# Performance work log

Hardware: AMD Instinct MI355X
Metric: run time of the kernel (lower is better)

## Reference

```python
import jax, jax.numpy as jnp
import numpy as np

DIM = 2048
N_HEADS = 16
Q_LORA = 1536
KV_LORA = 512
NOPE = 128
ROPE = 64
V_DIM = 128
B, T = 1, 3072
EPS = 1e-6


def rmsnorm(x, w):
    var = jnp.mean(jnp.square(x), axis=-1, keepdims=True)
    return x * jax.lax.rsqrt(var + EPS) * w


def apply_rope(x, cos, sin):
    # x: (B, T, H, d); cos/sin: (T, d//2) -> broadcast (1, T, 1, d//2)
    c = cos[None, :, None, :]
    s = sin[None, :, None, :]
    x1 = x[..., 0::2]
    x2 = x[..., 1::2]
    r1 = x1 * c - x2 * s
    r2 = x1 * s + x2 * c
    return jnp.stack([r1, r2], axis=-1).reshape(x.shape)


def setup_inputs() -> dict:
    key = jax.random.key(0)
    ks = jax.random.split(key, 10)
    std = 0.02
    x = jax.random.normal(ks[0], (B, T, DIM), dtype=jnp.float32)
    # RoPE angles: position * inv_freq, shape (T, ROPE//2)
    inv_freq = 1.0 / (10000.0 ** (np.arange(0, ROPE, 2, dtype=np.float32) / ROPE))
    freqs = jnp.asarray(np.arange(T, dtype=np.float32)[:, None] * inv_freq[None, :])
    # additive causal mask (T, T)
    mask = jnp.where(jnp.tril(jnp.ones((T, T), dtype=bool)), 0.0, -jnp.inf).astype(jnp.float32)
    wq_down = jax.random.normal(ks[1], (DIM, Q_LORA), dtype=jnp.float32) * std
    q_norm_w = jnp.ones((Q_LORA,), dtype=jnp.float32)
    wq_nope = jax.random.normal(ks[2], (Q_LORA, N_HEADS * NOPE), dtype=jnp.float32) * std
    wq_rope = jax.random.normal(ks[3], (Q_LORA, N_HEADS * ROPE), dtype=jnp.float32) * std
    wkv_down = jax.random.normal(ks[4], (DIM, KV_LORA + ROPE), dtype=jnp.float32) * std
    kv_norm_w = jnp.ones((KV_LORA,), dtype=jnp.float32)
    wkv_up = jax.random.normal(ks[5], (KV_LORA, N_HEADS * (NOPE + V_DIM)), dtype=jnp.float32) * std
    wo = jax.random.normal(ks[6], (N_HEADS * V_DIM, DIM), dtype=jnp.float32) * std
    return {
        'x': x, 'freqs': freqs, 'mask': mask,
        'wq_down': wq_down, 'q_norm_w': q_norm_w, 'wq_nope': wq_nope,
        'wq_rope': wq_rope, 'wkv_down': wkv_down, 'kv_norm_w': kv_norm_w,
        'wkv_up': wkv_up, 'wo': wo,
    }


def reference(x, freqs, mask, wq_down, q_norm_w, wq_nope, wq_rope,
              wkv_down, kv_norm_w, wkv_up, wo):
    cos, sin = jnp.cos(freqs), jnp.sin(freqs)
    # Q path: down-project, RMSNorm, split nope/rope heads
    q_lat = rmsnorm(x @ wq_down, q_norm_w)                      # (B,T,Q_LORA)
    q_nope = (q_lat @ wq_nope).reshape(B, T, N_HEADS, NOPE)
    q_rope = apply_rope((q_lat @ wq_rope).reshape(B, T, N_HEADS, ROPE), cos, sin)
    q = jnp.concatenate([q_nope, q_rope], axis=-1)              # (B,T,H,192)
    # KV path: joint down-projection -> latent c_kv + raw rope key
    kvd = x @ wkv_down                                          # (B,T,KV_LORA+ROPE)
    c_kv = kvd[..., :KV_LORA]
    k_rope_raw = kvd[..., KV_LORA:]                             # (B,T,ROPE)
    k_rope = jnp.broadcast_to(k_rope_raw[:, :, None, :], (B, T, N_HEADS, ROPE))
    k_rope = apply_rope(k_rope, cos, sin)
    kv_up = (rmsnorm(c_kv, kv_norm_w) @ wkv_up).reshape(B, T, N_HEADS, NOPE + V_DIM)
    k_nope = kv_up[..., :NOPE]
    v = kv_up[..., NOPE:]                                       # (B,T,H,V_DIM)
    k = jnp.concatenate([k_nope, k_rope], axis=-1)              # (B,T,H,192)
    scale = (NOPE + ROPE) ** (-0.5)
    attn = jnp.einsum('bqhd,bkhd->bhqk', q, k) * scale + mask[None, None]
    attn = jax.nn.softmax(attn, axis=-1)                        # dropout p=0 (eval)
    out = jnp.einsum('bhqk,bkhd->bqhd', attn, v).reshape(B, T, N_HEADS * V_DIM)
    return out @ wo                                             # (B,T,DIM)
```

## Files before the change

kernel.cpp:

```cpp
#include <hip/hip_runtime.h>
#include <hip/hip_bf16.h>

typedef __bf16 bf16_t;
typedef __bf16 bf16x8 __attribute__((ext_vector_type(8)));
typedef float f32x4 __attribute__((ext_vector_type(4)));

#define T_SEQ 3072
#define DIM 2048
#define NH 16
#define QLORA 1536
#define KVLORA 512
#define NOPE 128
#define ROPE 64
#define VDIM 128
#define HD 192
#define SCALE 0.07216878364870323f
#define CHUNK 12

#define T1KV_LD 2112
#define QNR_LD 3072

__device__ inline float wave_reduce_sum(float v) {
    #pragma unroll
    for (int off = 32; off > 0; off >>= 1) v += __shfl_down(v, off);
    return v;
}

__device__ inline float block_reduce_sum_256(float v) {
    __shared__ float red[4];
    int lane = threadIdx.x & 63, w = threadIdx.x >> 6;
    v = wave_reduce_sum(v);
    if (lane == 0) red[w] = v;
    __syncthreads();
    if (threadIdx.x == 0) red[0] = red[0] + red[1] + red[2] + red[3];
    __syncthreads();
    return red[0];
}

__device__ inline void glds16(const bf16_t* g, bf16_t* l) {
    __builtin_amdgcn_global_load_lds(
        (const __attribute__((address_space(1))) unsigned int*)g,
        (__attribute__((address_space(3))) unsigned int*)l, 16, 0, 0);
}

__global__ void f2b_kernel(const float* __restrict__ in, bf16_t* __restrict__ out, int n) {
    int i = (blockIdx.x * 256 + threadIdx.x) * 4;
    if (i < n) {
        float4 v = *(const float4*)&in[i];
        bf16_t o[4] = {(bf16_t)v.x, (bf16_t)v.y, (bf16_t)v.z, (bf16_t)v.w};
        *(uint2*)&out[i] = *(const uint2*)o;
    }
}

__global__ __launch_bounds__(256) void transp_kernel(
    const float* __restrict__ in, bf16_t* __restrict__ out, int K, int N)
{
    __shared__ float tile[32][33];
    int k0 = blockIdx.y * 32, n0 = blockIdx.x * 32;
    int tx = threadIdx.x & 31, ty = threadIdx.x >> 5;
    #pragma unroll
    for (int i = 0; i < 4; ++i)
        tile[ty + i * 8][tx] = in[(size_t)(k0 + ty + i * 8) * N + n0 + tx];
    __syncthreads();
    #pragma unroll
    for (int i = 0; i < 4; ++i)
        out[(size_t)(n0 + ty + i * 8) * K + k0 + tx] = (bf16_t)tile[tx][ty + i * 8];
}

__global__ __launch_bounds__(256) void vt_transp(
    const bf16_t* __restrict__ kvu, bf16_t* __restrict__ vt)
{
    __shared__ bf16_t tile[32][34];
    int t0 = blockIdx.x * 32, d0 = blockIdx.y * 32, h = blockIdx.z;
    int tx = threadIdx.x & 31, ty = threadIdx.x >> 5;
    #pragma unroll
    for (int i = 0; i < 4; ++i)
        tile[ty + i * 8][tx] = kvu[(size_t)(t0 + ty + i * 8) * (NH * 256) + h * 256 + NOPE + d0 + tx];
    __syncthreads();
    #pragma unroll
    for (int i = 0; i < 4; ++i)
        vt[((size_t)h * VDIM + d0 + ty + i * 8) * T_SEQ + t0 + tx] = tile[tx][ty + i * 8];
}

__global__ __launch_bounds__(256) void gemm_mfma(
    const bf16_t* __restrict__ A, const bf16_t* __restrict__ Bt,
    float* __restrict__ Cf, bf16_t* __restrict__ Cb,
    int M, int N, int K, int lda, int ldb, int ldc, int writef)
{
    __shared__ __align__(16) bf16_t As[2][128 * 32];
    __shared__ __align__(16) bf16_t Bs[2][128 * 32];
    int tid = threadIdx.x;
    int w = tid >> 6, lane = tid & 63;
    int quad = lane >> 4, l16 = lane & 15;
    int bm = blockIdx.y * 128, bn = blockIdx.x * 128;
    int wm = (w & 1) * 64, wn = (w >> 1) * 64;

    int srow = tid >> 2, soff = (tid & 3) * 8;
    const bf16_t* a0 = A + (size_t)(bm + srow) * lda + soff;
    const bf16_t* a1 = A + (size_t)(bm + 64 + srow) * lda + soff;
    int br0 = bn + srow;      if (br0 >= N) br0 = N - 1;
    int br1 = bn + 64 + srow; if (br1 >= N) br1 = N - 1;
    const bf16_t* b0 = Bt + (size_t)br0 * ldb + soff;
    const bf16_t* b1 = Bt + (size_t)br1 * ldb + soff;

    f32x4 acc[4][4];
    #pragma unroll
    for (int i = 0; i < 4; ++i)
        #pragma unroll
        for (int j = 0; j < 4; ++j)
            acc[i][j] = (f32x4){0.f, 0.f, 0.f, 0.f};

    int nk = K >> 5;
    glds16(a0, &As[0][tid * 8]);
    glds16(a1, &As[0][tid * 8 + 2048]);
    glds16(b0, &Bs[0][tid * 8]);
    glds16(b1, &Bs[0][tid * 8 + 2048]);
    a0 += 32; a1 += 32; b0 += 32; b1 += 32;

    for (int t = 0; t < nk; ++t) {
        int cur = t & 1;
        if (t + 1 < nk) {
            int nxt = cur ^ 1;
            glds16(a0, &As[nxt][tid * 8]);
            glds16(a1, &As[nxt][tid * 8 + 2048]);
            glds16(b0, &Bs[nxt][tid * 8]);
            glds16(b1, &Bs[nxt][tid * 8 + 2048]);
            a0 += 32; a1 += 32; b0 += 32; b1 += 32;
            asm volatile("s_waitcnt vmcnt(4)" ::: "memory");
        } else {
            asm volatile("s_waitcnt vmcnt(0)" ::: "memory");
        }
        __builtin_amdgcn_s_barrier();
        __builtin_amdgcn_sched_barrier(0);

        bf16x8 af[4], bfr[4];
        #pragma unroll
        for (int t4 = 0; t4 < 4; ++t4) {
            af[t4]  = *(const bf16x8*)&As[cur][(wm + t4 * 16 + l16) * 32 + quad * 8];
            bfr[t4] = *(const bf16x8*)&Bs[cur][(wn + t4 * 16 + l16) * 32 + quad * 8];
        }
        #pragma unroll
        for (int i = 0; i < 4; ++i)
            #pragma unroll
            for (int j = 0; j < 4; ++j)
                acc[i][j] = __builtin_amdgcn_mfma_f32_16x16x32_bf16(af[i], bfr[j], acc[i][j], 0, 0, 0);

        __builtin_amdgcn_sched_barrier(0);
        __builtin_amdgcn_s_barrier();
        __builtin_amdgcn_sched_barrier(0);
    }

    #pragma unroll
    for (int i = 0; i < 4; ++i) {
        #pragma unroll
        for (int j = 0; j < 4; ++j) {
            #pragma unroll
            for (int r = 0; r < 4; ++r) {
                int row = bm + wm + i * 16 + quad * 4 + r;
                int col = bn + wn + j * 16 + l16;
                if (col < N) {
                    if (writef) Cf[(size_t)row * ldc + col] = acc[i][j][r];
                    else        Cb[(size_t)row * ldc + col] = (bf16_t)acc[i][j][r];
                }
            }
        }
    }
}

__global__ __launch_bounds__(256) void rmsnorm_rows(
    bf16_t* __restrict__ X, const float* __restrict__ w, int N, int ld)
{
    int row = blockIdx.x;
    bf16_t* x = X + (size_t)row * ld;
    float ss = 0.f;
    for (int i = threadIdx.x; i < N; i += 256) { float v = (float)x[i]; ss += v * v; }
    ss = block_reduce_sum_256(ss);
    float sc = rsqrtf(ss / (float)N + 1e-6f);
    for (int i = threadIdx.x; i < N; i += 256)
        x[i] = (bf16_t)((float)x[i] * sc * w[i]);
}

__global__ __launch_bounds__(256) void kv_post(
    const bf16_t* __restrict__ kvd, const float* __restrict__ w,
    const float* __restrict__ freqs,
    bf16_t* __restrict__ ckvn, bf16_t* __restrict__ kr)
{
    int row = blockIdx.x;
    const bf16_t* src = kvd + (size_t)row * T1KV_LD;
    float ss = 0.f;
    for (int i = threadIdx.x; i < KVLORA; i += 256) { float v = (float)src[i]; ss += v * v; }
    ss = block_reduce_sum_256(ss);
    float sc = rsqrtf(ss / (float)KVLORA + 1e-6f);
    for (int i = threadIdx.x; i < KVLORA; i += 256)
        ckvn[(size_t)row * KVLORA + i] = (bf16_t)((float)src[i] * sc * w[i]);
    if (threadIdx.x < 32) {
        int i = threadIdx.x;
        float f = freqs[row * 32 + i];
        float c = cosf(f), s = sinf(f);
        float x1 = (float)src[KVLORA + 2 * i], x2 = (float)src[KVLORA + 2 * i + 1];
        kr[(size_t)row * ROPE + 2 * i]     = (bf16_t)(x1 * c - x2 * s);
        kr[(size_t)row * ROPE + 2 * i + 1] = (bf16_t)(x1 * s + x2 * c);
    }
}

__global__ void rope_q(bf16_t* __restrict__ qr, const float* __restrict__ freqs) {
    int idx = blockIdx.x * 256 + threadIdx.x;
    if (idx >= T_SEQ * NH * 32) return;
    int t = idx >> 9;
    int rem = idx & 511;
    int h = rem >> 5;
    int i = rem & 31;
    float f = freqs[t * 32 + i];
    float c = cosf(f), s = sinf(f);
    bf16_t* p = qr + (size_t)t * QNR_LD + h * ROPE + 2 * i;
    float x1 = (float)p[0], x2 = (float)p[1];
    p[0] = (bf16_t)(x1 * c - x2 * s);
    p[1] = (bf16_t)(x1 * s + x2 * c);
}

#define P_STRIDE 72
__global__ __launch_bounds__(256, 2) void attn_v10(
    const bf16_t* __restrict__ QNR,
    const bf16_t* __restrict__ KVU, const bf16_t* __restrict__ KR,
    const bf16_t* __restrict__ Vt,
    bf16_t* __restrict__ Opart, float* __restrict__ lpart)
{
    __shared__ __align__(16) bf16_t Kn[64 * 128];
    __shared__ __align__(16) bf16_t Kr[64 * 64];
    __shared__ __align__(16) bf16_t Vs[128 * 64];
    __shared__ __align__(16) bf16_t Ps[4][32 * P_STRIDE];

    int qt2 = blockIdx.x, cx = blockIdx.y, h = blockIdx.z;
    int ktmax = 2 * qt2 + 2;
    int kt0 = cx * CHUNK;
    if (kt0 >= ktmax) return;
    int kt1 = min(ktmax, kt0 + CHUNK);
    int g = qt2 / 6, r6 = qt2 - g * 6;
    int slot = h * 60 + 3 * g * (g + 1) + r6 * (g + 1) + cx;

    int tid = threadIdx.x;
    int w = tid >> 6, lane = tid & 63;
    int quad = lane >> 4, l16 = lane & 15;
    int qbase = qt2 * 128;

    bf16x8 qf[2][6];
    #pragma unroll
    for (int qs = 0; qs < 2; ++qs) {
        int qrow = qbase + qs * 64 + w * 16 + l16;
        #pragma unroll
        for (int kk = 0; kk < 4; ++kk)
            qf[qs][kk] = *(const bf16x8*)&QNR[(size_t)qrow * QNR_LD + h * NOPE + kk * 32 + quad * 8];
        #pragma unroll
        for (int kk = 4; kk < 6; ++kk)
            qf[qs][kk] = *(const bf16x8*)&QNR[(size_t)qrow * QNR_LD + (NH * NOPE) + h * ROPE + (kk - 4) * 32 + quad * 8];
    }

    int l4 = lane >> 4, l3 = lane >> 3;
    const bf16_t* kn_e = KVU + (size_t)(kt0 * 64 + w * 16 + l4) * (NH * 256) + h * 256 + ((lane & 15) ^ l4) * 8;
    const bf16_t* kn_o = KVU + (size_t)(kt0 * 64 + w * 16 + l4) * (NH * 256) + h * 256 + ((lane & 15) ^ (4 + l4)) * 8;
    const bf16_t* krp  = KR  + (size_t)(kt0 * 64 + w * 16 + l3) * ROPE + ((lane & 7) ^ l3) * 8;
    const bf16_t* vp   = Vt  + ((size_t)h * VDIM + w * 32 + l3) * T_SEQ + kt0 * 64 + ((lane & 7) ^ l3) * 8;

    bf16x8 ones;
    #pragma unroll
    for (int i = 0; i < 8; ++i) ones[i] = (bf16_t)1.0f;

    f32x4 o[2][8];
    #pragma unroll
    for (int qs = 0; qs < 2; ++qs)
        #pragma unroll
        for (int nt = 0; nt < 8; ++nt) o[qs][nt] = (f32x4){0.f, 0.f, 0.f, 0.f};
    f32x4 lacc[2];
    lacc[0] = (f32x4){0.f, 0.f, 0.f, 0.f};
    lacc[1] = (f32x4){0.f, 0.f, 0.f, 0.f};

    for (int kt = kt0; kt < kt1; ++kt) {
        int kbase = kt * 64;
        #pragma unroll
        for (int i = 0; i < 4; ++i)
            glds16(((i & 1) ? kn_o : kn_e) + (size_t)i * 4 * (NH * 256), &Kn[(w * 4 + i) * 512]);
        #pragma unroll
        for (int i = 0; i < 2; ++i)
            glds16(krp + (size_t)i * 8 * ROPE, &Kr[(w * 2 + i) * 512]);
        #pragma unroll
        for (int i = 0; i < 4; ++i)
            glds16(vp + (size_t)i * 8 * T_SEQ, &Vs[(w * 4 + i) * 512]);
        kn_e += (size_t)64 * NH * 256;
        kn_o += (size_t)64 * NH * 256;
        krp  += 64 * ROPE;
        vp   += 64;
        __syncthreads();

        f32x4 S[2][4];
        #pragma unroll
        for (int qs = 0; qs < 2; ++qs)
            #pragma unroll
            for (int c = 0; c < 4; ++c) S[qs][c] = (f32x4){0.f, 0.f, 0.f, 0.f};
        #pragma unroll
        for (int kk = 0; kk < 4; ++kk) {
            #pragma unroll
            for (int c = 0; c < 4; ++c) {
                bf16x8 kf = *(const bf16x8*)&Kn[(c * 16 + l16) * 128 + (((kk * 4 + quad) ^ (l16 & 7)) * 8)];
                S[0][c] = __builtin_amdgcn_mfma_f32_16x16x32_bf16(qf[0][kk], kf, S[0][c], 0, 0, 0);
                S[1][c] = __builtin_amdgcn_mfma_f32_16x16x32_bf16(qf[1][kk], kf, S[1][c], 0, 0, 0);
            }
        }
        #pragma unroll
        for (int kk = 4; kk < 6; ++kk) {
            #pragma unroll
            for (int c = 0; c < 4; ++c) {
                bf16x8 kf = *(const bf16x8*)&Kr[(c * 16 + l16) * 64 + ((((kk - 4) * 4 + quad) ^ (l16 & 7)) * 8)];
                S[0][c] = __builtin_amdgcn_mfma_f32_16x16x32_bf16(qf[0][kk], kf, S[0][c], 0, 0, 0);
                S[1][c] = __builtin_amdgcn_mfma_f32_16x16x32_bf16(qf[1][kk], kf, S[1][c], 0, 0, 0);
            }
        }

        #pragma unroll
        for (int qs = 0; qs < 2; ++qs) {
            #pragma unroll
            for (int c = 0; c < 4; ++c) {
                #pragma unroll
                for (int j = 0; j < 4; ++j) {
                    int col = kbase + c * 16 + l16;
                    int grow = qbase + qs * 64 + w * 16 + quad * 4 + j;
                    float p = (col <= grow) ? __expf(S[qs][c][j] * SCALE) : 0.f;
                    Ps[w][(qs * 16 + quad * 4 + j) * P_STRIDE + c * 16 + l16] = (bf16_t)p;
                }
            }
        }
        __asm__ volatile("s_waitcnt lgkmcnt(0)" ::: "memory");

        bf16x8 pf[2][2];
        #pragma unroll
        for (int qs = 0; qs < 2; ++qs) {
            pf[qs][0] = *(const bf16x8*)&Ps[w][(qs * 16 + l16) * P_STRIDE + quad * 8];
            pf[qs][1] = *(const bf16x8*)&Ps[w][(qs * 16 + l16) * P_STRIDE + 32 + quad * 8];
            lacc[qs] = __builtin_amdgcn_mfma_f32_16x16x32_bf16(pf[qs][0], ones, lacc[qs], 0, 0, 0);
            lacc[qs] = __builtin_amdgcn_mfma_f32_16x16x32_bf16(pf[qs][1], ones, lacc[qs], 0, 0, 0);
        }

        #pragma unroll
        for (int kk2 = 0; kk2 < 2; ++kk2) {
            #pragma unroll
            for (int nt = 0; nt < 8; ++nt) {
                bf16x8 vf = *(const bf16x8*)&Vs[(nt * 16 + l16) * 64 + (((kk2 * 4 + quad) ^ (l16 & 7)) * 8)];
                o[0][nt] = __builtin_amdgcn_mfma_f32_16x16x32_bf16(pf[0][kk2], vf, o[0][nt], 0, 0, 0);
                o[1][nt] = __builtin_amdgcn_mfma_f32_16x16x32_bf16(pf[1][kk2], vf, o[1][nt], 0, 0, 0);
            }
        }
        __syncthreads();
    }

    #pragma unroll
    for (int qs = 0; qs < 2; ++qs) {
        #pragma unroll
        for (int nt = 0; nt < 8; ++nt)
            #pragma unroll
            for (int j = 0; j < 4; ++j)
                Opart[(size_t)slot * 16384 + (qs * 64 + w * 16 + quad * 4 + j) * 128 + nt * 16 + l16] = (bf16_t)o[qs][nt][j];
        if (l16 == 0) {
            #pragma unroll
            for (int j = 0; j < 4; ++j)
                lpart[slot * 128 + qs * 64 + w * 16 + quad * 4 + j] = lacc[qs][j];
        }
    }
}

__global__ __launch_bounds__(512) void attn_combine(
    const bf16_t* __restrict__ Opart, const float* __restrict__ lpart,
    bf16_t* __restrict__ AO)
{
    int qt2 = blockIdx.x, h = blockIdx.y;
    int g = qt2 / 6, r6 = qt2 - g * 6;
    int nch = g + 1;
    int base = h * 60 + 3 * g * (g + 1) + r6 * (g + 1);
    int r = threadIdx.x >> 2, c0 = (threadIdx.x & 3) * 32;

    float acc[32];
    #pragma unroll
    for (int i = 0; i < 32; ++i) acc[i] = 0.f;
    float lsum = 0.f;
    for (int ch = 0; ch < nch; ++ch) {
        int slot = base + ch;
        const bf16_t* p = &Opart[(size_t)slot * 16384 + r * 128 + c0];
        #pragma unroll
        for (int v = 0; v < 4; ++v) {
            bf16x8 u = *(const bf16x8*)&p[v * 8];
            #pragma unroll
            for (int e = 0; e < 8; ++e) acc[v * 8 + e] += (float)u[e];
        }
        lsum += lpart[slot * 128 + r];
    }
    float inv = 1.0f / lsum;
    bf16_t* dst = AO + (size_t)(qt2 * 128 + r) * (NH * VDIM) + h * VDIM + c0;
    #pragma unroll
    for (int v = 0; v < 4; ++v) {
        bf16_t tmp[8];
        #pragma unroll
        for (int e = 0; e < 8; ++e) tmp[e] = (bf16_t)(acc[v * 8 + e] * inv);
        *(uint4*)&dst[v * 8] = *(const uint4*)tmp;
    }
}

extern "C" void kernel_launch(void* const* d_in, const int* in_sizes, int n_in,
                              void* d_out, int out_size, void* d_ws, size_t ws_size,
                              hipStream_t stream) {
    const float* x        = (const float*)d_in[0];
    const float* freqs    = (const float*)d_in[1];
    const float* wq_down  = (const float*)d_in[3];
    const float* q_norm_w = (const float*)d_in[4];
    const float* wq_nope  = (const float*)d_in[5];
    const float* wq_rope  = (const float*)d_in[6];
    const float* wkv_down = (const float*)d_in[7];
    const float* kv_norm_w= (const float*)d_in[8];
    const float* wkv_up   = (const float*)d_in[9];
    const float* wo       = (const float*)d_in[10];
    float* out = (float*)d_out;

    bf16_t* ws = (bf16_t*)d_ws;
    bf16_t* xb     = ws;
    bf16_t* wqd_t  = xb     + 6291456;
    bf16_t* wkvd_t = wqd_t  + 3145728;
    bf16_t* wqn_t  = wkvd_t + 1179648;
    bf16_t* wqr_t  = wqn_t  + 3145728;
    bf16_t* wkvu_t = wqr_t  + 1572864;
    bf16_t* t1kv   = wkvu_t + 2097152;
    bf16_t* ckvn   = t1kv   + 6488064;
    bf16_t* Opart  = ws;
    float*  lpart  = (float*)(ws + 15728640);
    bf16_t* ao     = ws + 15728640 + 245760;
    bf16_t* wo_t   = ws    + 25493504;
    bf16_t* kr     = wo_t  + 4194304;
    bf16_t* qnr    = kr    + 196608;
    bf16_t* kvu    = qnr   + 9437184;
    bf16_t* vt     = kvu   + 12582912;

    f2b_kernel<<<T_SEQ * DIM / 4 / 256, 256, 0, stream>>>(x, xb, T_SEQ * DIM);
    transp_kernel<<<dim3(QLORA / 32, DIM / 32), 256, 0, stream>>>(wq_down, wqd_t, DIM, QLORA);
    transp_kernel<<<dim3((KVLORA + ROPE) / 32, DIM / 32), 256, 0, stream>>>(wkv_down, wkvd_t, DIM, KVLORA + ROPE);
    transp_kernel<<<dim3(NH * NOPE / 32, QLORA / 32), 256, 0, stream>>>(wq_nope, wqn_t, QLORA, NH * NOPE);
    transp_kernel<<<dim3(NH * ROPE / 32, QLORA / 32), 256, 0, stream>>>(wq_rope, wqr_t, QLORA, NH * ROPE);
    transp_kernel<<<dim3(NH * 256 / 32, KVLORA / 32), 256, 0, stream>>>(wkv_up, wkvu_t, KVLORA, NH * 256);
    transp_kernel<<<dim3(DIM / 32, DIM / 32), 256, 0, stream>>>(wo, wo_t, DIM, DIM);

    gemm_mfma<<<dim3(17, T_SEQ / 128), 256, 0, stream>>>(
        xb, wqd_t, nullptr, t1kv, T_SEQ, 2112, DIM, DIM, DIM, T1KV_LD, 0);

    rmsnorm_rows<<<T_SEQ, 256, 0, stream>>>(t1kv, q_norm_w, QLORA, T1KV_LD);
    kv_post<<<T_SEQ, 256, 0, stream>>>(t1kv + QLORA, kv_norm_w, freqs, ckvn, kr);

    gemm_mfma<<<dim3(24, T_SEQ / 128), 256, 0, stream>>>(
        t1kv, wqn_t, nullptr, qnr, T_SEQ, 3072, QLORA, T1KV_LD, QLORA, QNR_LD, 0);
    rope_q<<<(T_SEQ * NH * 32 + 255) / 256, 256, 0, stream>>>(qnr + NH * NOPE, freqs);

    gemm_mfma<<<dim3(NH * 256 / 128, T_SEQ / 128), 256, 0, stream>>>(
        ckvn, wkvu_t, nullptr, kvu, T_SEQ, NH * 256, KVLORA, KVLORA, KVLORA, NH * 256, 0);

    vt_transp<<<dim3(T_SEQ / 32, VDIM / 32, NH), 256, 0, stream>>>(kvu, vt);

    attn_v10<<<dim3(T_SEQ / 128, 4, NH), 256, 0, stream>>>(qnr, kvu, kr, vt, Opart, lpart);
    attn_combine<<<dim3(T_SEQ / 128, NH), 512, 0, stream>>>(Opart, lpart, ao);

    gemm_mfma<<<dim3(DIM / 128, T_SEQ / 128), 256, 0, stream>>>(
        ao, wo_t, out, nullptr, T_SEQ, DIM, DIM, DIM, DIM, DIM, 1);
}
```

Before: 483.4 us.

## Double-buffer attention K/V tiles with 32-key steps and async prefetch

Rewrites the attention kernel to use 32-key tiles instead of 64, held in two shared-memory buffers. The next tile is prefetched with direct global-to-LDS loads while the current one is computed, and explicit vmcnt waits and raw barriers replace __syncthreads. The aim is to hide global load latency behind the MFMA work. The cost is twice as many loop iterations and barriers, smaller MFMA batches per step, and the occupancy hint of 2 blocks per CU is dropped.

```diff
diff --git a/kernel.cpp b/kernel.cpp
--- a/kernel.cpp
+++ b/kernel.cpp
@@ -15,7 +15,6 @@
 #define VDIM 128
 #define HD 192
 #define SCALE 0.07216878364870323f
-#define CHUNK 12
 
 #define T1KV_LD 2112
 #define QNR_LD 3072
@@ -218,23 +217,23 @@
     p[1] = (bf16_t)(x1 * s + x2 * c);
 }
 
-#define P_STRIDE 72
-__global__ __launch_bounds__(256, 2) void attn_v10(
+#define PS_STRIDE 40
+__global__ __launch_bounds__(256) void attn_v11(
     const bf16_t* __restrict__ QNR,
     const bf16_t* __restrict__ KVU, const bf16_t* __restrict__ KR,
     const bf16_t* __restrict__ Vt,
     bf16_t* __restrict__ Opart, float* __restrict__ lpart)
 {
-    __shared__ __align__(16) bf16_t Kn[64 * 128];
-    __shared__ __align__(16) bf16_t Kr[64 * 64];
-    __shared__ __align__(16) bf16_t Vs[128 * 64];
-    __shared__ __align__(16) bf16_t Ps[4][32 * P_STRIDE];
+    __shared__ __align__(16) bf16_t Kn[2][32 * 128];
+    __shared__ __align__(16) bf16_t Kr[2][32 * 64];
+    __shared__ __align__(16) bf16_t Vs[2][128 * 32];
+    __shared__ __align__(16) bf16_t Ps[4][32 * PS_STRIDE];
 
     int qt2 = blockIdx.x, cx = blockIdx.y, h = blockIdx.z;
-    int ktmax = 2 * qt2 + 2;
-    int kt0 = cx * CHUNK;
+    int ktmax = 4 * qt2 + 4;
+    int kt0 = cx * 24;
     if (kt0 >= ktmax) return;
-    int kt1 = min(ktmax, kt0 + CHUNK);
+    int kt1 = min(ktmax, kt0 + 24);
     int g = qt2 / 6, r6 = qt2 - g * 6;
     int slot = h * 60 + 3 * g * (g + 1) + r6 * (g + 1) + cx;
 
@@ -255,11 +254,13 @@
             qf[qs][kk] = *(const bf16x8*)&QNR[(size_t)qrow * QNR_LD + (NH * NOPE) + h * ROPE + (kk - 4) * 32 + quad * 8];
     }
 
-    int l4 = lane >> 4, l3 = lane >> 3;
-    const bf16_t* kn_e = KVU + (size_t)(kt0 * 64 + w * 16 + l4) * (NH * 256) + h * 256 + ((lane & 15) ^ l4) * 8;
-    const bf16_t* kn_o = KVU + (size_t)(kt0 * 64 + w * 16 + l4) * (NH * 256) + h * 256 + ((lane & 15) ^ (4 + l4)) * 8;
-    const bf16_t* krp  = KR  + (size_t)(kt0 * 64 + w * 16 + l3) * ROPE + ((lane & 7) ^ l3) * 8;
-    const bf16_t* vp   = Vt  + ((size_t)h * VDIM + w * 32 + l3) * T_SEQ + kt0 * 64 + ((lane & 7) ^ l3) * 8;
+    int l4 = lane >> 4, l3 = lane >> 3, l2 = lane >> 2;
+    const bf16_t* kn0 = KVU + (size_t)(kt0 * 32 + w * 8 + l4) * (NH * 256) + h * 256 + ((lane & 15) ^ l4) * 8;
+    const bf16_t* kn1 = KVU + (size_t)(kt0 * 32 + w * 8 + 4 + l4) * (NH * 256) + h * 256 + ((lane & 15) ^ (4 + l4)) * 8;
+    const bf16_t* krp = KR + (size_t)(kt0 * 32 + w * 8 + l3) * ROPE + ((lane & 7) ^ l3) * 8;
+    int vswz = (l2 >> 1) & 3;
+    const bf16_t* vp0 = Vt + ((size_t)h * VDIM + w * 32 + l2) * T_SEQ + kt0 * 32 + ((lane & 3) ^ vswz) * 8;
+    const bf16_t* vp1 = Vt + ((size_t)h * VDIM + w * 32 + 16 + l2) * T_SEQ + kt0 * 32 + ((lane & 3) ^ vswz) * 8;
 
     bf16x8 ones;
     #pragma unroll
@@ -274,33 +275,43 @@
     lacc[0] = (f32x4){0.f, 0.f, 0.f, 0.f};
     lacc[1] = (f32x4){0.f, 0.f, 0.f, 0.f};
 
+    glds16(kn0, &Kn[0][(w * 2 + 0) * 512]);
+    glds16(kn1, &Kn[0][(w * 2 + 1) * 512]);
+    glds16(krp, &Kr[0][w * 512]);
+    glds16(vp0, &Vs[0][(w * 2 + 0) * 512]);
+    glds16(vp1, &Vs[0][(w * 2 + 1) * 512]);
+    kn0 += (size_t)32 * NH * 256; kn1 += (size_t)32 * NH * 256;
+    krp += 32 * ROPE; vp0 += 32; vp1 += 32;
+
     for (int kt = kt0; kt < kt1; ++kt) {
-        int kbase = kt * 64;
-        #pragma unroll
-        for (int i = 0; i < 4; ++i)
-            glds16(((i & 1) ? kn_o : kn_e) + (size_t)i * 4 * (NH * 256), &Kn[(w * 4 + i) * 512]);
-        #pragma unroll
-        for (int i = 0; i < 2; ++i)
-            glds16(krp + (size_t)i * 8 * ROPE, &Kr[(w * 2 + i) * 512]);
-        #pragma unroll
-        for (int i = 0; i < 4; ++i)
-            glds16(vp + (size_t)i * 8 * T_SEQ, &Vs[(w * 4 + i) * 512]);
-        kn_e += (size_t)64 * NH * 256;
-        kn_o += (size_t)64 * NH * 256;
-        krp  += 64 * ROPE;
-        vp   += 64;
-        __syncthreads();
-
-        f32x4 S[2][4];
+        int kbase = kt * 32;
+        int cur = (kt - kt0) & 1;
+        if (kt + 1 < kt1) {
+            int nxt = cur ^ 1;
+            glds16(kn0, &Kn[nxt][(w * 2 + 0) * 512]);
+            glds16(kn1, &Kn[nxt][(w * 2 + 1) * 512]);
+            glds16(krp, &Kr[nxt][w * 512]);
+            glds16(vp0, &Vs[nxt][(w * 2 + 0) * 512]);
+            glds16(vp1, &Vs[nxt][(w * 2 + 1) * 512]);
+            kn0 += (size_t)32 * NH * 256; kn1 += (size_t)32 * NH * 256;
+            krp += 32 * ROPE; vp0 += 32; vp1 += 32;
+            asm volatile("s_waitcnt vmcnt(5)" ::: "memory");
+        } else {
+            asm volatile("s_waitcnt vmcnt(0)" ::: "memory");
+        }
+        __builtin_amdgcn_s_barrier();
+        __builtin_amdgcn_sched_barrier(0);
+
+        f32x4 S[2][2];
         #pragma unroll
         for (int qs = 0; qs < 2; ++qs)
             #pragma unroll
-            for (int c = 0; c < 4; ++c) S[qs][c] = (f32x4){0.f, 0.f, 0.f, 0.f};
+            for (int c = 0; c < 2; ++c) S[qs][c] = (f32x4){0.f, 0.f, 0.f, 0.f};
         #pragma unroll
         for (int kk = 0; kk < 4; ++kk) {
             #pragma unroll
-            for (int c = 0; c < 4; ++c) {
-                bf16x8 kf = *(const bf16x8*)&Kn[(c * 16 + l16) * 128 + (((kk * 4 + quad) ^ (l16 & 7)) * 8)];
+            for (int c = 0; c < 2; ++c) {
+                bf16x8 kf = *(const bf16x8*)&Kn[cur][(c * 16 + l16) * 128 + (((kk * 4 + quad) ^ (l16 & 7)) * 8)];
                 S[0][c] = __builtin_amdgcn_mfma_f32_16x16x32_bf16(qf[0][kk], kf, S[0][c], 0, 0, 0);
                 S[1][c] = __builtin_amdgcn_mfma_f32_16x16x32_bf16(qf[1][kk], kf, S[1][c], 0, 0, 0);
             }
@@ -308,8 +319,8 @@
         #pragma unroll
         for (int kk = 4; kk < 6; ++kk) {
             #pragma unroll
-            for (int c = 0; c < 4; ++c) {
-                bf16x8 kf = *(const bf16x8*)&Kr[(c * 16 + l16) * 64 + ((((kk - 4) * 4 + quad) ^ (l16 & 7)) * 8)];
+            for (int c = 0; c < 2; ++c) {
+                bf16x8 kf = *(const bf16x8*)&Kr[cur][(c * 16 + l16) * 64 + ((((kk - 4) * 4 + quad) ^ (l16 & 7)) * 8)];
                 S[0][c] = __builtin_amdgcn_mfma_f32_16x16x32_bf16(qf[0][kk], kf, S[0][c], 0, 0, 0);
                 S[1][c] = __builtin_amdgcn_mfma_f32_16x16x32_bf16(qf[1][kk], kf, S[1][c], 0, 0, 0);
             }
@@ -318,37 +329,34 @@
         #pragma unroll
         for (int qs = 0; qs < 2; ++qs) {
             #pragma unroll
-            for (int c = 0; c < 4; ++c) {
+            for (int c = 0; c < 2; ++c) {
                 #pragma unroll
                 for (int j = 0; j < 4; ++j) {
                     int col = kbase + c * 16 + l16;
                     int grow = qbase + qs * 64 + w * 16 + quad * 4 + j;
                     float p = (col <= grow) ? __expf(S[qs][c][j] * SCALE) : 0.f;
-                    Ps[w][(qs * 16 + quad * 4 + j) * P_STRIDE + c * 16 + l16] = (bf16_t)p;
+                    Ps[w][(qs * 16 + quad * 4 + j) * PS_STRIDE + c * 16 + l16] = (bf16_t)p;
                 }
             }
         }
         __asm__ volatile("s_waitcnt lgkmcnt(0)" ::: "memory");
 
-        bf16x8 pf[2][2];
+        bf16x8 pf[2];
         #pragma unroll
         for (int qs = 0; qs < 2; ++qs) {
-            pf[qs][0] = *(const bf16x8*)&Ps[w][(qs * 16 + l16) * P_STRIDE + quad * 8];
-            pf[qs][1] = *(const bf16x8*)&Ps[w][(qs * 16 + l16) * P_STRIDE + 32 + quad * 8];
-            lacc[qs] = __builtin_amdgcn_mfma_f32_16x16x32_bf16(pf[qs][0], ones, lacc[qs], 0, 0, 0);
-            lacc[qs] = __builtin_amdgcn_mfma_f32_16x16x32_bf16(pf[qs][1], ones, lacc[qs], 0, 0, 0);
-        }
-
-        #pragma unroll
-        for (int kk2 = 0; kk2 < 2; ++kk2) {
-            #pragma unroll
-            for (int nt = 0; nt < 8; ++nt) {
-                bf16x8 vf = *(const bf16x8*)&Vs[(nt * 16 + l16) * 64 + (((kk2 * 4 + quad) ^ (l16 & 7)) * 8)];
-                o[0][nt] = __builtin_amdgcn_mfma_f32_16x16x32_bf16(pf[0][kk2], vf, o[0][nt], 0, 0, 0);
-                o[1][nt] = __builtin_amdgcn_mfma_f32_16x16x32_bf16(pf[1][kk2], vf, o[1][nt], 0, 0, 0);
-            }
-        }
-        __syncthreads();
+            pf[qs] = *(const bf16x8*)&Ps[w][(qs * 16 + l16) * PS_STRIDE + quad * 8];
+            lacc[qs] = __builtin_amdgcn_mfma_f32_16x16x32_bf16(pf[qs], ones, lacc[qs], 0, 0, 0);
+        }
+
+        #pragma unroll
+        for (int nt = 0; nt < 8; ++nt) {
+            bf16x8 vf = *(const bf16x8*)&Vs[cur][(nt * 16 + l16) * 32 + ((quad ^ ((l16 >> 1) & 3)) * 8)];
+            o[0][nt] = __builtin_amdgcn_mfma_f32_16x16x32_bf16(pf[0], vf, o[0][nt], 0, 0, 0);
+            o[1][nt] = __builtin_amdgcn_mfma_f32_16x16x32_bf16(pf[1], vf, o[1][nt], 0, 0, 0);
+        }
+        __builtin_amdgcn_sched_barrier(0);
+        __builtin_amdgcn_s_barrier();
+        __builtin_amdgcn_sched_barrier(0);
     }
 
     #pragma unroll
@@ -458,7 +466,7 @@
 
     vt_transp<<<dim3(T_SEQ / 32, VDIM / 32, NH), 256, 0, stream>>>(kvu, vt);
 
-    attn_v10<<<dim3(T_SEQ / 128, 4, NH), 256, 0, stream>>>(qnr, kvu, kr, vt, Opart, lpart);
+    attn_v11<<<dim3(T_SEQ / 128, 4, NH), 256, 0, stream>>>(qnr, kvu, kr, vt, Opart, lpart);
     attn_combine<<<dim3(T_SEQ / 128, NH), 512, 0, stream>>>(Opart, lpart, ao);
 
     gemm_mfma<<<dim3(DIM / 128, T_SEQ / 128), 256, 0, stream>>>(
```

Measured after the change: 506.5 us. 4.8% more time.
